# Optimization experiments

Hardware: AMD Instinct MI355X
Metric: run time of the kernel (lower is better)

## Reference

```python
import jax, jax.numpy as jnp
import numpy as np


def setup_inputs() -> dict:
    key = jax.random.key(0)
    B, C, N = 1, 8, 320
    n_shots, spp = 4, 1502
    inp = jax.random.normal(key, (B, C, N, N, 2), dtype=jnp.float32)
    # radial trajectory initialization, faithful to initilaize_trajectory('radial')
    theta = np.pi / n_shots
    L = np.arange(-160, 160, 320.0 / spp, dtype=np.float32)[:spp]
    traj = np.zeros((n_shots, spp, 2), dtype=np.float32)
    for i in range(n_shots):
        traj[i, :, 0] = L * np.cos(theta * i)
        traj[i, :, 1] = L * np.sin(theta * i)
    return {"inp": inp, "traj": jnp.asarray(traj)}


def _nufft_roundtrip(inp, traj):
    # inp: [B, C, H, W, 2] real/imag pairs; traj: [n_shots, spp, 2] in [-N/2, N/2)
    N = inp.shape[2]
    img = (inp[..., 0] + 1j * inp[..., 1]).astype(jnp.complex64)  # [B,C,H,W]
    xf = traj.reshape(-1, 2)                                      # [M,2]
    kx, ky = xf[:, 0], xf[:, 1]
    grid = (jnp.arange(N) - N // 2).astype(jnp.float32)           # centered pixel coords
    w = jnp.complex64(-2j * jnp.pi / N)
    Ax = jnp.exp(w * (kx[:, None] * grid[None, :])).astype(jnp.complex64)  # [M,H]
    Ay = jnp.exp(w * (ky[:, None] * grid[None, :])).astype(jnp.complex64)  # [M,W]
    # type-2 NUFFT (exact nonuniform DFT): image -> nonuniform k-space samples
    t = jnp.einsum('mx,bcxy->bcmy', Ax, img)        # [B,C,M,W]
    ksp = jnp.einsum('bcmy,my->bcm', t, Ay)         # [B,C,M]
    # adjoint (type-1): nonuniform samples -> Cartesian image grid
    tmp = ksp[..., None] * jnp.conj(Ay)[None, None]  # [B,C,M,W]
    out = jnp.einsum('mx,bcmw->bcxw', jnp.conj(Ax), tmp)  # [B,C,H,W]
    return jnp.stack([out.real, out.imag], axis=-1)  # [B,C,H,W,2]


def reference(inp, traj):
    return _nufft_roundtrip(inp, traj)
```

## Files before the change

### kernel.cpp

```cpp
#include <hip/hip_runtime.h>
#include <math.h>


#define NN      320
#define BCC     8
#define MREAL   6008
#define MSTR    6144
#define MT1     47
#define P1STR   6016
#define SKADJ   8
#define CHUNKM  (MSTR / SKADJ)
#define NADJB   (SKADJ * BCC * 25)
#define TWOPI   6.283185307179586f

typedef __attribute__((ext_vector_type(8))) short short8_t;
typedef __attribute__((ext_vector_type(4))) float float4_t;

__device__ __forceinline__ unsigned short f2bf(float f) {
    union { float f; unsigned u; } v; v.f = f;
    unsigned r = v.u + 0x7fff + ((v.u >> 16) & 1);
    return (unsigned short)(r >> 16);
}
__device__ __forceinline__ float bf2f(unsigned short h) {
    union { unsigned u; float f; } v; v.u = ((unsigned)h) << 16;
    return v.f;
}
__device__ __forceinline__ short8_t neg8(short8_t v) {
    short8_t r;
    #pragma unroll
    for (int i = 0; i < 8; ++i) r[i] = v[i] ^ (short)0x8000;
    return r;
}
__device__ __forceinline__ float gval(int i) { return (float)(i - NN/2); }

__device__ __forceinline__ void phase_cs(float k, float g, float* c, float* s) {
    float rev = k * (g * (1.0f / (float)NN));
    rev -= rintf(rev);
    float th = rev * TWOPI;
    __sincosf(th, s, c);
}

__device__ __forceinline__ void gld16(const unsigned short* g, unsigned short* l) {
    __builtin_amdgcn_global_load_lds(
        (const __attribute__((address_space(1))) unsigned int*)g,
        (__attribute__((address_space(3))) unsigned int*)l, 16, 0, 0);
}

__global__ __launch_bounds__(256) void gen_A(
    const float* __restrict__ traj,
    unsigned short* __restrict__ Ax_r, unsigned short* __restrict__ Ax_i,
    unsigned short* __restrict__ AxT_r, unsigned short* __restrict__ AxT_i,
    unsigned short* __restrict__ AyT_r, unsigned short* __restrict__ AyT_i)
{
    __shared__ __align__(16) float lc[64][65];
    __shared__ __align__(16) float ls[64][65];
    __shared__ float kxv[64], kyv[64];
    const int tid = threadIdx.x;
    const int m0 = blockIdx.x * 64;
    const int g0 = blockIdx.y * 64;

    if (tid < 64) {
        int m = m0 + tid;
        kxv[tid] = (m < MREAL) ? traj[2*m]     : 0.f;
        kyv[tid] = (m < MREAL) ? traj[2*m + 1] : 0.f;
    }
    __syncthreads();

    #pragma unroll
    for (int it = 0; it < 16; ++it) {
        int e = tid + it * 256;
        int mi = e >> 6, gi = e & 63;
        float c, s;
        phase_cs(kxv[mi], gval(g0 + gi), &c, &s);
        bool valid = (m0 + mi) < MREAL;
        lc[mi][gi] = valid ? c : 0.f;
        ls[mi][gi] = valid ? s : 0.f;
    }
    __syncthreads();
    #pragma unroll
    for (int it = 0; it < 16; ++it) {
        int e = tid + it * 256;
        int mi = e >> 6, xi = e & 63;
        int m = m0 + mi;
        size_t o = (size_t)m * NN + g0 + (xi ^ ((m & 7) << 3));
        Ax_r[o] = f2bf(lc[mi][xi]);
        Ax_i[o] = f2bf(-ls[mi][xi]);
    }
    #pragma unroll
    for (int it = 0; it < 16; ++it) {
        int e = tid + it * 256;
        int xi = e >> 6, mi = e & 63;
        int x = g0 + xi;
        size_t o = (size_t)x * MSTR + m0 + (mi ^ ((x & 7) << 3));
        AxT_r[o] = f2bf(lc[mi][xi]);
        AxT_i[o] = f2bf(ls[mi][xi]);
    }
    __syncthreads();

    #pragma unroll
    for (int it = 0; it < 16; ++it) {
        int e = tid + it * 256;
        int mi = e >> 6, gi = e & 63;
        float c, s;
        phase_cs(kyv[mi], gval(g0 + gi), &c, &s);
        bool valid = (m0 + mi) < MREAL;
        lc[mi][gi] = valid ? c : 0.f;
        ls[mi][gi] = valid ? s : 0.f;
    }
    __syncthreads();
    #pragma unroll
    for (int it = 0; it < 16; ++it) {
        int e = tid + it * 256;
        int yi = e >> 6, mi = e & 63;
        size_t o = (size_t)(g0 + yi) * MSTR + (m0 + mi);
        AyT_r[o] = f2bf(lc[mi][yi]);
        AyT_i[o] = f2bf(ls[mi][yi]);
    }
}

__global__ __launch_bounds__(256) void conv_img(
    const float* __restrict__ inp,
    unsigned short* __restrict__ iT_r, unsigned short* __restrict__ iT_i)
{
    __shared__ __align__(16) float2 t[64][65];
    const int tid = threadIdx.x;
    const int x0 = blockIdx.x * 64, y0 = blockIdx.y * 64, bc = blockIdx.z;
    const float2* ip = (const float2*)inp;
    #pragma unroll
    for (int it = 0; it < 16; ++it) {
        int e = tid + it * 256;
        int r = e >> 6, c = e & 63;
        t[r][c] = ip[((size_t)bc * NN + (x0 + r)) * NN + (y0 + c)];
    }
    __syncthreads();
    #pragma unroll
    for (int it = 0; it < 16; ++it) {
        int e = tid + it * 256;
        int yy = e >> 6, xx = e & 63;
        float2 v = t[xx][yy];
        int y = y0 + yy;
        size_t o = ((size_t)bc * NN + y) * NN + x0 + (xx ^ ((y & 7) << 3));
        iT_r[o] = f2bf(v.x);
        iT_i[o] = f2bf(v.y);
    }
}

__global__ __launch_bounds__(256) void fwd_gemm(
    const unsigned short* __restrict__ iT_r, const unsigned short* __restrict__ iT_i,
    const unsigned short* __restrict__ Ax_r, const unsigned short* __restrict__ Ax_i,
    const unsigned short* __restrict__ AyT_r, const unsigned short* __restrict__ AyT_i,
    float2* __restrict__ partial1)
{
    __shared__ __align__(16) unsigned short ST[24576];
    __shared__ __align__(16) float2 redbuf[2][128];

    const int tid = threadIdx.x;
    const int bid = blockIdx.x;
    const int nid = (bid & 7) * 235 + (bid >> 3);
    const int mt  = nid / 40;
    const int r40 = nid - mt * 40;
    const int yt  = r40 % 5;
    const int bc  = r40 / 5;
    const int m0  = mt * 128;
    const int y0  = yt * 64;

    float4_t accR[2][4], accI[2][4];
    #pragma unroll
    for (int i = 0; i < 2; ++i)
        #pragma unroll
        for (int j = 0; j < 4; ++j) { accR[i][j] = (float4_t)0.f; accI[i][j] = (float4_t)0.f; }

    const int lane = tid & 63, wid = tid >> 6;
    const int wy = wid & 1, wm = wid >> 1;
    const int ar = lane & 15, kb = lane >> 4;
    const int sxor = (lane & 7) << 3;

    const int lrow = lane >> 3;
    const int cb8  = (lane & 7) * 8;

    for (int x0i = 0; x0i < NN; x0i += 64) {
        for (int s = wid; s < 48; s += 4) {
            const unsigned short* g;
            if (s < 16) {
                int row = (s & 7) * 8 + lrow;
                const unsigned short* pl = (s < 8) ? iT_r : iT_i;
                g = pl + ((size_t)bc * NN + (y0 + row)) * NN + x0i + cb8;
            } else {
                int row = ((s - 16) & 15) * 8 + lrow;
                const unsigned short* pl = (s < 32) ? Ax_r : Ax_i;
                g = pl + (size_t)(m0 + row) * NN + x0i + cb8;
            }
            gld16(g, &ST[s * 512]);
        }
        __syncthreads();

        #pragma unroll
        for (int ks = 0; ks < 2; ++ks) {
            const int e = (ks * 32 + kb * 8) ^ sxor;
            short8_t a_r[2], a_i[2], a_n[2], b_r[4], b_i[4];
            #pragma unroll
            for (int iy = 0; iy < 2; ++iy) {
                int rr = wy * 32 + iy * 16 + ar;
                a_r[iy] = *(const short8_t*)&ST[rr * 64 + e];
                a_i[iy] = *(const short8_t*)&ST[4096 + rr * 64 + e];
                a_n[iy] = neg8(a_i[iy]);
            }
            #pragma unroll
            for (int jm = 0; jm < 4; ++jm) {
                int cc = wm * 64 + jm * 16 + ar;
                b_r[jm] = *(const short8_t*)&ST[8192  + cc * 64 + e];
                b_i[jm] = *(const short8_t*)&ST[16384 + cc * 64 + e];
            }
            #pragma unroll
            for (int iy = 0; iy < 2; ++iy)
                #pragma unroll
                for (int jm = 0; jm < 4; ++jm) {
                    accR[iy][jm] = __builtin_amdgcn_mfma_f32_16x16x32_bf16(a_r[iy], b_r[jm], accR[iy][jm], 0, 0, 0);
                    accR[iy][jm] = __builtin_amdgcn_mfma_f32_16x16x32_bf16(a_n[iy], b_i[jm], accR[iy][jm], 0, 0, 0);
                    accI[iy][jm] = __builtin_amdgcn_mfma_f32_16x16x32_bf16(a_r[iy], b_i[jm], accI[iy][jm], 0, 0, 0);
                    accI[iy][jm] = __builtin_amdgcn_mfma_f32_16x16x32_bf16(a_i[iy], b_r[jm], accI[iy][jm], 0, 0, 0);
                }
        }
        __syncthreads();
    }

    #pragma unroll
    for (int jm = 0; jm < 4; ++jm) {
        float sr = 0.f, si = 0.f;
        int m = m0 + wm * 64 + jm * 16 + ar;
        #pragma unroll
        for (int iy = 0; iy < 2; ++iy)
            #pragma unroll
            for (int q = 0; q < 4; ++q) {
                int y = y0 + wy * 32 + iy * 16 + kb * 4 + q;
                float c  = bf2f(AyT_r[(size_t)y * MSTR + m]);
                float sy = bf2f(AyT_i[(size_t)y * MSTR + m]);
                float Tr = accR[iy][jm][q], Ti = accI[iy][jm][q];
                sr += Tr * c + Ti * sy;
                si += Ti * c - Tr * sy;
            }
        sr += __shfl_xor(sr, 16); sr += __shfl_xor(sr, 32);
        si += __shfl_xor(si, 16); si += __shfl_xor(si, 32);
        if ((lane & 48) == 0)
            redbuf[wy][wm * 64 + jm * 16 + ar] = make_float2(sr, si);
    }
    __syncthreads();
    if (tid < 128) {
        float2 a = redbuf[0][tid], b = redbuf[1][tid];
        int m = m0 + tid;
        if (m < MREAL)
            partial1[((size_t)bc * 5 + yt) * P1STR + m] = make_float2(a.x + b.x, a.y + b.y);
    }
}

__global__ void reduce_ksp(const float2* __restrict__ partial1,
                           float2* __restrict__ ksp)
{
    int mp = blockIdx.x * 256 + threadIdx.x;
    int bc = blockIdx.y;
    float2 r = make_float2(0.f, 0.f);
    if (mp < MREAL) {
        #pragma unroll
        for (int yt = 0; yt < 5; ++yt) {
            float2 v = partial1[((size_t)bc * 5 + yt) * P1STR + mp];
            r.x += v.x; r.y += v.y;
        }
    }
    ksp[(size_t)bc * MSTR + mp] = r;
}

__global__ __launch_bounds__(256) void gen_U(
    const unsigned short* __restrict__ AyT_r, const unsigned short* __restrict__ AyT_i,
    const float2* __restrict__ ksp,
    unsigned short* __restrict__ U_r, unsigned short* __restrict__ U_i)
{
    const int tid = threadIdx.x;
    const int m0 = blockIdx.x * 2048 + tid * 8;
    const int y  = blockIdx.y;
    const int bc = blockIdx.z;

    short8_t yr = *(const short8_t*)(AyT_r + (size_t)y * MSTR + m0);
    short8_t yi = *(const short8_t*)(AyT_i + (size_t)y * MSTR + m0);
    const float2* kp = ksp + (size_t)bc * MSTR + m0;
    short8_t ur, ui;
    #pragma unroll
    for (int j = 0; j < 8; ++j) {
        float2 k = kp[j];
        float cr = bf2f((unsigned short)yr[j]);
        float ci = bf2f((unsigned short)yi[j]);
        ur[j] = (short)f2bf(k.x * cr - k.y * ci);
        ui[j] = (short)f2bf(k.x * ci + k.y * cr);
    }
    size_t o = ((size_t)bc * NN + y) * MSTR + (m0 ^ ((y & 7) << 3));
    *(short8_t*)(U_r + o) = ur;
    *(short8_t*)(U_i + o) = ui;
}

template<int FP32P>
__global__ __launch_bounds__(256) void adj_gemm_pre(
    const unsigned short* __restrict__ AxT_r, const unsigned short* __restrict__ AxT_i,
    const unsigned short* __restrict__ U_r, const unsigned short* __restrict__ U_i,
    void* __restrict__ partial2)
{
    __shared__ __align__(16) unsigned short ST[16384];

    const int tid = threadIdx.x;
    const int bid = blockIdx.x;
    const int nid = (bid & 7) * (NADJB / 8) + (bid >> 3);
    const int bcsk = nid / 25;
    const int xy = nid - bcsk * 25;
    const int xt = xy / 5, yt = xy % 5;
    const int bc = bcsk % BCC, sk = bcsk / BCC;
    const int x0 = xt * 64, y0 = yt * 64;
    const int kbeg = sk * CHUNKM;

    float4_t accR[2][2], accI[2][2];
    #pragma unroll
    for (int i = 0; i < 2; ++i)
        #pragma unroll
        for (int j = 0; j < 2; ++j) { accR[i][j] = (float4_t)0.f; accI[i][j] = (float4_t)0.f; }

    const int lane = tid & 63, wid = tid >> 6;
    const int wx = wid >> 1, wyy = wid & 1;
    const int ar = lane & 15, kb = lane >> 4;
    const int sxor = (lane & 7) << 3;

    const int lrow = lane >> 3;
    const int cb8  = (lane & 7) * 8;

    for (int mk = 0; mk < CHUNKM; mk += 64) {
        for (int s = wid; s < 32; s += 4) {
            int row = (s & 7) * 8 + lrow;
            const unsigned short* g;
            if (s < 16) {
                const unsigned short* pl = (s < 8) ? AxT_r : AxT_i;
                g = pl + (size_t)(x0 + row) * MSTR + kbeg + mk + cb8;
            } else {
                const unsigned short* pl = (s < 24) ? U_r : U_i;
                g = pl + ((size_t)bc * NN + (y0 + row)) * MSTR + kbeg + mk + cb8;
            }
            gld16(g, &ST[s * 512]);
        }
        __syncthreads();

        #pragma unroll
        for (int ks = 0; ks < 2; ++ks) {
            const int e = (ks * 32 + kb * 8) ^ sxor;
            short8_t a_r[2], a_i[2], a_n[2], b_r[2], b_i[2];
            #pragma unroll
            for (int ix = 0; ix < 2; ++ix) {
                int rr = wx * 32 + ix * 16 + ar;
                a_r[ix] = *(const short8_t*)&ST[rr * 64 + e];
                a_i[ix] = *(const short8_t*)&ST[4096 + rr * 64 + e];
                a_n[ix] = neg8(a_i[ix]);
            }
            #pragma unroll
            for (int jy = 0; jy < 2; ++jy) {
                int cc = wyy * 32 + jy * 16 + ar;
                b_r[jy] = *(const short8_t*)&ST[8192  + cc * 64 + e];
                b_i[jy] = *(const short8_t*)&ST[12288 + cc * 64 + e];
            }
            #pragma unroll
            for (int ix = 0; ix < 2; ++ix)
                #pragma unroll
                for (int jy = 0; jy < 2; ++jy) {
                    accR[ix][jy] = __builtin_amdgcn_mfma_f32_16x16x32_bf16(a_r[ix], b_r[jy], accR[ix][jy], 0, 0, 0);
                    accR[ix][jy] = __builtin_amdgcn_mfma_f32_16x16x32_bf16(a_n[ix], b_i[jy], accR[ix][jy], 0, 0, 0);
                    accI[ix][jy] = __builtin_amdgcn_mfma_f32_16x16x32_bf16(a_r[ix], b_i[jy], accI[ix][jy], 0, 0, 0);
                    accI[ix][jy] = __builtin_amdgcn_mfma_f32_16x16x32_bf16(a_i[ix], b_r[jy], accI[ix][jy], 0, 0, 0);
                }
        }
        __syncthreads();
    }

    #pragma unroll
    for (int ix = 0; ix < 2; ++ix)
        #pragma unroll
        for (int jy = 0; jy < 2; ++jy)
            #pragma unroll
            for (int q = 0; q < 4; ++q) {
                int x = x0 + wx * 32 + ix * 16 + kb * 4 + q;
                int y = y0 + wyy * 32 + jy * 16 + ar;
                size_t o = (((size_t)sk * BCC + bc) * NN + x) * NN + y;
                float vr = accR[ix][jy][q], vi = accI[ix][jy][q];
                if (FP32P) {
                    ((float2*)partial2)[o] = make_float2(vr, vi);
                } else {
                    ((unsigned*)partial2)[o] =
                        (unsigned)f2bf(vr) | ((unsigned)f2bf(vi) << 16);
                }
            }
}

template<int FP32P>
__global__ __launch_bounds__(256) void adj_gemm_fb(
    const unsigned short* __restrict__ AxT_r, const unsigned short* __restrict__ AxT_i,
    const unsigned short* __restrict__ AyT_r, const unsigned short* __restrict__ AyT_i,
    const float2* __restrict__ ksp, void* __restrict__ partial2)
{
    __shared__ __align__(16) unsigned short Ar[64][72], Ai[64][72];
    __shared__ __align__(16) unsigned short Br[64][72], Bi[64][72];
    __shared__ __align__(16) float2 kspl[CHUNKM];

    const int tid = threadIdx.x;
    const int bid = blockIdx.x;
    const int nid = (bid & 7) * (NADJB / 8) + (bid >> 3);
    const int bcsk = nid / 25;
    const int xy = nid - bcsk * 25;
    const int xt = xy / 5, yt = xy % 5;
    const int bc = bcsk % BCC, sk = bcsk / BCC;
    const int x0 = xt * 64, y0 = yt * 64;
    const int kbeg = sk * CHUNKM;

    #pragma unroll
    for (int it = 0; it < CHUNKM / 256; ++it)
        kspl[tid + it * 256] = ksp[(size_t)bc * MSTR + kbeg + tid + it * 256];
    __syncthreads();

    float4_t accR[2][2], accI[2][2];
    #pragma unroll
    for (int i = 0; i < 2; ++i)
        #pragma unroll
        for (int j = 0; j < 2; ++j) { accR[i][j] = (float4_t)0.f; accI[i][j] = (float4_t)0.f; }

    const int lane = tid & 63, wid = tid >> 6;
    const int wx = wid >> 1, wyy = wid & 1;
    const int ar = lane & 15, kb = lane >> 4;
    const int sxor = (lane & 7) << 3;

    for (int mk = 0; mk < CHUNKM; mk += 64) {
        #pragma unroll
        for (int it = 0; it < 2; ++it) {
            int e = tid + it * 256;
            int row = e >> 3, gr = e & 7;
            size_t o = (size_t)(x0 + row) * MSTR + kbeg + mk + gr * 8;
            *(short8_t*)&Ar[row][gr * 8] = *(const short8_t*)(AxT_r + o);
            *(short8_t*)&Ai[row][gr * 8] = *(const short8_t*)(AxT_i + o);
        }
        #pragma unroll
        for (int it = 0; it < 2; ++it) {
            int e = tid + it * 256;
            int row = e >> 3, gr = e & 7;
            size_t o = (size_t)(y0 + row) * MSTR + kbeg + mk + gr * 8;
            short8_t yr = *(const short8_t*)(AyT_r + o);
            short8_t yi = *(const short8_t*)(AyT_i + o);
            short8_t br, bi2;
            #pragma unroll
            for (int j = 0; j < 8; ++j) {
                float2 k = kspl[mk + gr * 8 + j];
                float cr = bf2f((unsigned short)yr[j]);
                float ci = bf2f((unsigned short)yi[j]);
                br[j]  = (short)f2bf(k.x * cr - k.y * ci);
                bi2[j] = (short)f2bf(k.x * ci + k.y * cr);
            }
            *(short8_t*)&Br[row][gr * 8] = br;
            *(short8_t*)&Bi[row][gr * 8] = bi2;
        }
        __syncthreads();

        #pragma unroll
        for (int ks = 0; ks < 2; ++ks) {
            const int ea = (ks * 32 + kb * 8) ^ sxor;
            const int eb = ks * 32 + kb * 8;
            short8_t a_r[2], a_i[2], a_n[2], b_r[2], b_i[2];
            #pragma unroll
            for (int ix = 0; ix < 2; ++ix) {
                int rr = wx * 32 + ix * 16 + ar;
                a_r[ix] = *(const short8_t*)&Ar[rr][ea];
                a_i[ix] = *(const short8_t*)&Ai[rr][ea];
                a_n[ix] = neg8(a_i[ix]);
            }
            #pragma unroll
            for (int jy = 0; jy < 2; ++jy) {
                int cc = wyy * 32 + jy * 16 + ar;
                b_r[jy] = *(const short8_t*)&Br[cc][eb];
                b_i[jy] = *(const short8_t*)&Bi[cc][eb];
            }
            #pragma unroll
            for (int ix = 0; ix < 2; ++ix)
                #pragma unroll
                for (int jy = 0; jy < 2; ++jy) {
                    accR[ix][jy] = __builtin_amdgcn_mfma_f32_16x16x32_bf16(a_r[ix], b_r[jy], accR[ix][jy], 0, 0, 0);
                    accR[ix][jy] = __builtin_amdgcn_mfma_f32_16x16x32_bf16(a_n[ix], b_i[jy], accR[ix][jy], 0, 0, 0);
                    accI[ix][jy] = __builtin_amdgcn_mfma_f32_16x16x32_bf16(a_r[ix], b_i[jy], accI[ix][jy], 0, 0, 0);
                    accI[ix][jy] = __builtin_amdgcn_mfma_f32_16x16x32_bf16(a_i[ix], b_r[jy], accI[ix][jy], 0, 0, 0);
                }
        }
        __syncthreads();
    }

    #pragma unroll
    for (int ix = 0; ix < 2; ++ix)
        #pragma unroll
        for (int jy = 0; jy < 2; ++jy)
            #pragma unroll
            for (int q = 0; q < 4; ++q) {
                int x = x0 + wx * 32 + ix * 16 + kb * 4 + q;
                int y = y0 + wyy * 32 + jy * 16 + ar;
                size_t o = (((size_t)sk * BCC + bc) * NN + x) * NN + y;
                float vr = accR[ix][jy][q], vi = accI[ix][jy][q];
                if (FP32P) {
                    ((float2*)partial2)[o] = make_float2(vr, vi);
                } else {
                    ((unsigned*)partial2)[o] =
                        (unsigned)f2bf(vr) | ((unsigned)f2bf(vi) << 16);
                }
            }
}

template<int FP32P>
__global__ void reduce_out(const void* __restrict__ partial2,
                           float2* __restrict__ out)
{
    size_t total = (size_t)BCC * NN * NN;
    size_t idx = (size_t)blockIdx.x * 256 + threadIdx.x;
    if (idx >= total) return;
    float2 r = make_float2(0.f, 0.f);
    #pragma unroll
    for (int s = 0; s < SKADJ; ++s) {
        if (FP32P) {
            float2 v = ((const float2*)partial2)[s * total + idx];
            r.x += v.x; r.y += v.y;
        } else {
            unsigned u = ((const unsigned*)partial2)[s * total + idx];
            r.x += bf2f((unsigned short)(u & 0xffff));
            r.y += bf2f((unsigned short)(u >> 16));
        }
    }
    out[idx] = r;
}

extern "C" void kernel_launch(void* const* d_in, const int* in_sizes, int n_in,
                              void* d_out, int out_size, void* d_ws, size_t ws_size,
                              hipStream_t stream)
{
    const float* inp  = (const float*)d_in[0];
    const float* traj = (const float*)d_in[1];

    char* ws = (char*)d_ws;
    const size_t PL = (size_t)NN * MSTR * 2;
    unsigned short* AxT_r = (unsigned short*)(ws);
    unsigned short* AxT_i = (unsigned short*)(ws + PL);
    unsigned short* AyT_r = (unsigned short*)(ws + 2 * PL);
    unsigned short* AyT_i = (unsigned short*)(ws + 3 * PL);
    float2* ksp = (float2*)(ws + 4 * PL);
    const size_t KSPB = (size_t)BCC * MSTR * 8;
    const size_t BASE = 4 * PL + KSPB;
    char* rb = ws + BASE;
    unsigned short* Ax_r = (unsigned short*)(rb);
    unsigned short* Ax_i = (unsigned short*)(rb + PL);
    const size_t ITP = (size_t)BCC * NN * NN * 2;
    unsigned short* iT_r = (unsigned short*)(rb + 2 * PL);
    unsigned short* iT_i = (unsigned short*)(rb + 2 * PL + ITP);
    float2* partial1 = (float2*)(rb + 2 * PL + 2 * ITP);
    const size_t UPL = (size_t)BCC * NN * MSTR * 2;
    unsigned short* U_r = (unsigned short*)(rb);
    unsigned short* U_i = (unsigned short*)(rb + UPL);
    const size_t ADJ_F32 = (size_t)SKADJ * BCC * NN * NN * 8;
    const size_t ADJ_B16 = ADJ_F32 / 2;

    gen_A<<<dim3(96, 5), 256, 0, stream>>>(traj, Ax_r, Ax_i, AxT_r, AxT_i, AyT_r, AyT_i);
    conv_img<<<dim3(5, 5, BCC), 256, 0, stream>>>(inp, iT_r, iT_i);
    fwd_gemm<<<dim3(1880), 256, 0, stream>>>(iT_r, iT_i, Ax_r, Ax_i, AyT_r, AyT_i, partial1);
    reduce_ksp<<<dim3(24, BCC), 256, 0, stream>>>(partial1, ksp);

    size_t total = (size_t)BCC * NN * NN;
    int rblocks = (int)((total + 255) / 256);

    if (ws_size >= BASE + 2 * UPL + ADJ_F32) {
        void* partial2 = (void*)(rb + 2 * UPL);
        gen_U<<<dim3(3, NN, BCC), 256, 0, stream>>>(AyT_r, AyT_i, ksp, U_r, U_i);
        adj_gemm_pre<1><<<dim3(NADJB), 256, 0, stream>>>(AxT_r, AxT_i, U_r, U_i, partial2);
        reduce_out<1><<<rblocks, 256, 0, stream>>>(partial2, (float2*)d_out);
    } else if (ws_size >= BASE + 2 * UPL + ADJ_B16) {
        void* partial2 = (void*)(rb + 2 * UPL);
        gen_U<<<dim3(3, NN, BCC), 256, 0, stream>>>(AyT_r, AyT_i, ksp, U_r, U_i);
        adj_gemm_pre<0><<<dim3(NADJB), 256, 0, stream>>>(AxT_r, AxT_i, U_r, U_i, partial2);
        reduce_out<0><<<rblocks, 256, 0, stream>>>(partial2, (float2*)d_out);
    } else if (ws_size >= BASE + ADJ_F32) {
        void* partial2 = (void*)rb;
        adj_gemm_fb<1><<<dim3(NADJB), 256, 0, stream>>>(AxT_r, AxT_i, AyT_r, AyT_i, ksp, partial2);
        reduce_out<1><<<rblocks, 256, 0, stream>>>(partial2, (float2*)d_out);
    } else {
        void* partial2 = (void*)rb;
        adj_gemm_fb<0><<<dim3(NADJB), 256, 0, stream>>>(AxT_r, AxT_i, AyT_r, AyT_i, ksp, partial2);
        reduce_out<0><<<rblocks, 256, 0, stream>>>(partial2, (float2*)d_out);
    }
}
```

Before: 158.6 us.

## Double-buffer LDS in forward/adjoint GEMMs, read image from global, prefer bf16 partials

```diff
diff --git a/kernel.cpp b/kernel.cpp
--- a/kernel.cpp
+++ b/kernel.cpp
@@ -138,8 +138,7 @@
         int e = tid + it * 256;
         int yy = e >> 6, xx = e & 63;
         float2 v = t[xx][yy];
-        int y = y0 + yy;
-        size_t o = ((size_t)bc * NN + y) * NN + x0 + (xx ^ ((y & 7) << 3));
+        size_t o = ((size_t)bc * NN + (y0 + yy)) * NN + (x0 + xx);
         iT_r[o] = f2bf(v.x);
         iT_i[o] = f2bf(v.y);
     }
@@ -151,7 +150,7 @@
     const unsigned short* __restrict__ AyT_r, const unsigned short* __restrict__ AyT_i,
     float2* __restrict__ partial1)
 {
-    __shared__ __align__(16) unsigned short ST[24576];
+    __shared__ __align__(16) unsigned short ST[2][16384];
     __shared__ __align__(16) float2 redbuf[2][128];
 
     const int tid = threadIdx.x;
@@ -178,51 +177,65 @@
     const int lrow = lane >> 3;
     const int cb8  = (lane & 7) * 8;
 
-    for (int x0i = 0; x0i < NN; x0i += 64) {
-        for (int s = wid; s < 48; s += 4) {
-            const unsigned short* g;
-            if (s < 16) {
-                int row = (s & 7) * 8 + lrow;
-                const unsigned short* pl = (s < 8) ? iT_r : iT_i;
-                g = pl + ((size_t)bc * NN + (y0 + row)) * NN + x0i + cb8;
-            } else {
-                int row = ((s - 16) & 15) * 8 + lrow;
-                const unsigned short* pl = (s < 32) ? Ax_r : Ax_i;
-                g = pl + (size_t)(m0 + row) * NN + x0i + cb8;
-            }
-            gld16(g, &ST[s * 512]);
-        }
-        __syncthreads();
-
-        #pragma unroll
-        for (int ks = 0; ks < 2; ++ks) {
-            const int e = (ks * 32 + kb * 8) ^ sxor;
-            short8_t a_r[2], a_i[2], a_n[2], b_r[4], b_i[4];
-            #pragma unroll
-            for (int iy = 0; iy < 2; ++iy) {
-                int rr = wy * 32 + iy * 16 + ar;
-                a_r[iy] = *(const short8_t*)&ST[rr * 64 + e];
-                a_i[iy] = *(const short8_t*)&ST[4096 + rr * 64 + e];
-                a_n[iy] = neg8(a_i[iy]);
-            }
-            #pragma unroll
-            for (int jm = 0; jm < 4; ++jm) {
-                int cc = wm * 64 + jm * 16 + ar;
-                b_r[jm] = *(const short8_t*)&ST[8192  + cc * 64 + e];
-                b_i[jm] = *(const short8_t*)&ST[16384 + cc * 64 + e];
-            }
-            #pragma unroll
-            for (int iy = 0; iy < 2; ++iy)
-                #pragma unroll
-                for (int jm = 0; jm < 4; ++jm) {
-                    accR[iy][jm] = __builtin_amdgcn_mfma_f32_16x16x32_bf16(a_r[iy], b_r[jm], accR[iy][jm], 0, 0, 0);
-                    accR[iy][jm] = __builtin_amdgcn_mfma_f32_16x16x32_bf16(a_n[iy], b_i[jm], accR[iy][jm], 0, 0, 0);
-                    accI[iy][jm] = __builtin_amdgcn_mfma_f32_16x16x32_bf16(a_r[iy], b_i[jm], accI[iy][jm], 0, 0, 0);
-                    accI[iy][jm] = __builtin_amdgcn_mfma_f32_16x16x32_bf16(a_i[iy], b_r[jm], accI[iy][jm], 0, 0, 0);
-                }
-        }
-        __syncthreads();
-    }
+    const unsigned short* gp[8];
+    #pragma unroll
+    for (int j = 0; j < 8; ++j) {
+        int s = wid + 4 * j;
+        int row = (s & 15) * 8 + lrow;
+        const unsigned short* pl = (s < 16) ? Ax_r : Ax_i;
+        gp[j] = pl + (size_t)(m0 + row) * NN + cb8;
+    }
+
+    const unsigned short* aR[2];
+    const unsigned short* aI[2];
+    #pragma unroll
+    for (int iy = 0; iy < 2; ++iy) {
+        size_t o = ((size_t)bc * NN + (y0 + wy * 32 + iy * 16 + ar)) * NN + kb * 8;
+        aR[iy] = iT_r + o;
+        aI[iy] = iT_i + o;
+    }
+
+#define FSTG(CUR) { _Pragma("unroll") \
+    for (int j = 0; j < 8; ++j) { gld16(gp[j], &ST[CUR][(wid + 4 * j) * 512]); gp[j] += 64; } }
+
+#define FCMP(CUR) { \
+    _Pragma("unroll") \
+    for (int ks = 0; ks < 2; ++ks) { \
+        const int e = (ks * 32 + kb * 8) ^ sxor; \
+        short8_t a_r[2], a_i[2], a_n[2], b_r[4], b_i[4]; \
+        _Pragma("unroll") \
+        for (int iy = 0; iy < 2; ++iy) { \
+            a_r[iy] = *(const short8_t*)(aR[iy] + ks * 32); \
+            a_i[iy] = *(const short8_t*)(aI[iy] + ks * 32); \
+            a_n[iy] = neg8(a_i[iy]); \
+        } \
+        _Pragma("unroll") \
+        for (int jm = 0; jm < 4; ++jm) { \
+            int cc = wm * 64 + jm * 16 + ar; \
+            b_r[jm] = *(const short8_t*)&ST[CUR][cc * 64 + e]; \
+            b_i[jm] = *(const short8_t*)&ST[CUR][8192 + cc * 64 + e]; \
+        } \
+        _Pragma("unroll") \
+        for (int iy = 0; iy < 2; ++iy) \
+            _Pragma("unroll") \
+            for (int jm = 0; jm < 4; ++jm) { \
+                accR[iy][jm] = __builtin_amdgcn_mfma_f32_16x16x32_bf16(a_r[iy], b_r[jm], accR[iy][jm], 0, 0, 0); \
+                accR[iy][jm] = __builtin_amdgcn_mfma_f32_16x16x32_bf16(a_n[iy], b_i[jm], accR[iy][jm], 0, 0, 0); \
+                accI[iy][jm] = __builtin_amdgcn_mfma_f32_16x16x32_bf16(a_r[iy], b_i[jm], accI[iy][jm], 0, 0, 0); \
+                accI[iy][jm] = __builtin_amdgcn_mfma_f32_16x16x32_bf16(a_i[iy], b_r[jm], accI[iy][jm], 0, 0, 0); \
+            } \
+    } \
+    _Pragma("unroll") \
+    for (int iy = 0; iy < 2; ++iy) { aR[iy] += 64; aI[iy] += 64; } }
+
+    FSTG(0); __syncthreads();
+    FSTG(1); FCMP(0); __syncthreads();
+    FSTG(0); FCMP(1); __syncthreads();
+    FSTG(1); FCMP(0); __syncthreads();
+    FSTG(0); FCMP(1); __syncthreads();
+    FCMP(0);
+#undef FSTG
+#undef FCMP
 
     #pragma unroll
     for (int jm = 0; jm < 4; ++jm) {
@@ -302,7 +315,7 @@
     const unsigned short* __restrict__ U_r, const unsigned short* __restrict__ U_i,
     void* __restrict__ partial2)
 {
-    __shared__ __align__(16) unsigned short ST[16384];
+    __shared__ __align__(16) unsigned short AST[2][16384];
 
     const int tid = threadIdx.x;
     const int bid = blockIdx.x;
@@ -328,50 +341,63 @@
     const int lrow = lane >> 3;
     const int cb8  = (lane & 7) * 8;
 
-    for (int mk = 0; mk < CHUNKM; mk += 64) {
-        for (int s = wid; s < 32; s += 4) {
-            int row = (s & 7) * 8 + lrow;
-            const unsigned short* g;
-            if (s < 16) {
-                const unsigned short* pl = (s < 8) ? AxT_r : AxT_i;
-                g = pl + (size_t)(x0 + row) * MSTR + kbeg + mk + cb8;
-            } else {
-                const unsigned short* pl = (s < 24) ? U_r : U_i;
-                g = pl + ((size_t)bc * NN + (y0 + row)) * MSTR + kbeg + mk + cb8;
-            }
-            gld16(g, &ST[s * 512]);
+    const unsigned short* gp[8];
+    #pragma unroll
+    for (int j = 0; j < 8; ++j) {
+        int s = wid + 4 * j;
+        int row = (s & 7) * 8 + lrow;
+        const unsigned short* g;
+        if (s < 16) {
+            const unsigned short* pl = (s < 8) ? AxT_r : AxT_i;
+            g = pl + (size_t)(x0 + row) * MSTR + kbeg + cb8;
+        } else {
+            const unsigned short* pl = (s < 24) ? U_r : U_i;
+            g = pl + ((size_t)bc * NN + (y0 + row)) * MSTR + kbeg + cb8;
         }
-        __syncthreads();
-
-        #pragma unroll
-        for (int ks = 0; ks < 2; ++ks) {
-            const int e = (ks * 32 + kb * 8) ^ sxor;
-            short8_t a_r[2], a_i[2], a_n[2], b_r[2], b_i[2];
-            #pragma unroll
-            for (int ix = 0; ix < 2; ++ix) {
-                int rr = wx * 32 + ix * 16 + ar;
-                a_r[ix] = *(const short8_t*)&ST[rr * 64 + e];
-                a_i[ix] = *(const short8_t*)&ST[4096 + rr * 64 + e];
-                a_n[ix] = neg8(a_i[ix]);
-            }
-            #pragma unroll
-            for (int jy = 0; jy < 2; ++jy) {
-                int cc = wyy * 32 + jy * 16 + ar;
-                b_r[jy] = *(const short8_t*)&ST[8192  + cc * 64 + e];
-                b_i[jy] = *(const short8_t*)&ST[12288 + cc * 64 + e];
-            }
-            #pragma unroll
-            for (int ix = 0; ix < 2; ++ix)
-                #pragma unroll
-                for (int jy = 0; jy < 2; ++jy) {
-                    accR[ix][jy] = __builtin_amdgcn_mfma_f32_16x16x32_bf16(a_r[ix], b_r[jy], accR[ix][jy], 0, 0, 0);
-                    accR[ix][jy] = __builtin_amdgcn_mfma_f32_16x16x32_bf16(a_n[ix], b_i[jy], accR[ix][jy], 0, 0, 0);
-                    accI[ix][jy] = __builtin_amdgcn_mfma_f32_16x16x32_bf16(a_r[ix], b_i[jy], accI[ix][jy], 0, 0, 0);
-                    accI[ix][jy] = __builtin_amdgcn_mfma_f32_16x16x32_bf16(a_i[ix], b_r[jy], accI[ix][jy], 0, 0, 0);
-                }
-        }
-        __syncthreads();
-    }
+        gp[j] = g;
+    }
+
+#define ASTG(CUR) { _Pragma("unroll") \
+    for (int j = 0; j < 8; ++j) { gld16(gp[j], &AST[CUR][(wid + 4 * j) * 512]); gp[j] += 64; } }
+
+#define ACMP(CUR) { \
+    _Pragma("unroll") \
+    for (int ks = 0; ks < 2; ++ks) { \
+        const int e = (ks * 32 + kb * 8) ^ sxor; \
+        short8_t a_r[2], a_i[2], a_n[2], b_r[2], b_i[2]; \
+        _Pragma("unroll") \
+        for (int ix = 0; ix < 2; ++ix) { \
+            int rr = wx * 32 + ix * 16 + ar; \
+            a_r[ix] = *(const short8_t*)&AST[CUR][rr * 64 + e]; \
+            a_i[ix] = *(const short8_t*)&AST[CUR][4096 + rr * 64 + e]; \
+            a_n[ix] = neg8(a_i[ix]); \
+        } \
+        _Pragma("unroll") \
+        for (int jy = 0; jy < 2; ++jy) { \
+            int cc = wyy * 32 + jy * 16 + ar; \
+            b_r[jy] = *(const short8_t*)&AST[CUR][8192  + cc * 64 + e]; \
+            b_i[jy] = *(const short8_t*)&AST[CUR][12288 + cc * 64 + e]; \
+        } \
+        _Pragma("unroll") \
+        for (int ix = 0; ix < 2; ++ix) \
+            _Pragma("unroll") \
+            for (int jy = 0; jy < 2; ++jy) { \
+                accR[ix][jy] = __builtin_amdgcn_mfma_f32_16x16x32_bf16(a_r[ix], b_r[jy], accR[ix][jy], 0, 0, 0); \
+                accR[ix][jy] = __builtin_amdgcn_mfma_f32_16x16x32_bf16(a_n[ix], b_i[jy], accR[ix][jy], 0, 0, 0); \
+                accI[ix][jy] = __builtin_amdgcn_mfma_f32_16x16x32_bf16(a_r[ix], b_i[jy], accI[ix][jy], 0, 0, 0); \
+                accI[ix][jy] = __builtin_amdgcn_mfma_f32_16x16x32_bf16(a_i[ix], b_r[jy], accI[ix][jy], 0, 0, 0); \
+            } \
+    } }
+
+    ASTG(0); __syncthreads();
+    #pragma unroll
+    for (int tt = 0; tt < 6; ++tt) {
+        ASTG(1); ACMP(0); __syncthreads();
+        if (tt < 5) ASTG(0);
+        ACMP(1); __syncthreads();
+    }
+#undef ASTG
+#undef ACMP
 
     #pragma unroll
     for (int ix = 0; ix < 2; ++ix)
@@ -567,12 +593,7 @@
     size_t total = (size_t)BCC * NN * NN;
     int rblocks = (int)((total + 255) / 256);
 
-    if (ws_size >= BASE + 2 * UPL + ADJ_F32) {
-        void* partial2 = (void*)(rb + 2 * UPL);
-        gen_U<<<dim3(3, NN, BCC), 256, 0, stream>>>(AyT_r, AyT_i, ksp, U_r, U_i);
-        adj_gemm_pre<1><<<dim3(NADJB), 256, 0, stream>>>(AxT_r, AxT_i, U_r, U_i, partial2);
-        reduce_out<1><<<rblocks, 256, 0, stream>>>(partial2, (float2*)d_out);
-    } else if (ws_size >= BASE + 2 * UPL + ADJ_B16) {
+    if (ws_size >= BASE + 2 * UPL + ADJ_B16) {
         void* partial2 = (void*)(rb + 2 * UPL);
         gen_U<<<dim3(3, NN, BCC), 256, 0, stream>>>(AyT_r, AyT_i, ksp, U_r, U_i);
         adj_gemm_pre<0><<<dim3(NADJB), 256, 0, stream>>>(AxT_r, AxT_i, U_r, U_i, partial2);
```

New measurement: 174.4 us. +9.9%, slower.
